# Kernel optimization log

Measured on AMD Instinct MI355X. Metric: run time of the kernel, lower is better.

## Reference

```python
import jax, jax.numpy as jnp
import numpy as np

N, E = 100000, 1600000
F_IN, H, HG, L, C = 128, 128, 128, 3, 40


def setup_inputs() -> dict:
    key = jax.random.key(0)
    ks = jax.random.split(key, 12)
    s = 0.05
    return dict(
        x=jax.random.normal(ks[0], (N, F_IN), jnp.float32),
        edge_index=jax.random.randint(ks[1], (2, E), 0, N),
        edge_weight=jax.random.uniform(ks[2], (E,), jnp.float32),
        h0=jax.random.normal(ks[3], (N, HG), jnp.float32),
        linW=jax.random.normal(ks[4], (F_IN, H), jnp.float32) * s,
        linB=jnp.zeros((H,), jnp.float32),
        convW=jax.random.normal(ks[5], (L, H, H), jnp.float32) * s,
        convB=jnp.zeros((L, H), jnp.float32),
        gru_Wih=jax.random.normal(ks[6], (3 * HG, H), jnp.float32) * s,
        gru_Whh=jax.random.normal(ks[7], (3 * HG, HG), jnp.float32) * s,
        gru_bih=jnp.zeros((3 * HG,), jnp.float32),
        gru_bhh=jnp.zeros((3 * HG,), jnp.float32),
        fcW=jax.random.normal(ks[8], (HG, C), jnp.float32) * s,
        fcB=jnp.zeros((C,), jnp.float32),
    )


def _gru(x, h, Wih, Whh, bih, bhh):
    # torch.nn.GRUCell math (gate order: r, z, n)
    gi = x @ Wih.T + bih  # [N, 3*HG]
    gh = h @ Whh.T + bhh  # [N, 3*HG]
    ir, iz, in_ = jnp.split(gi, 3, axis=-1)
    hr, hz, hn = jnp.split(gh, 3, axis=-1)
    r = jax.nn.sigmoid(ir + hr)
    z = jax.nn.sigmoid(iz + hz)
    n = jnp.tanh(in_ + r * hn)
    return (1.0 - z) * n + z * h


def _gcn_conv(x, src, dst, ew, W, b, n_nodes):
    # PyG GCNConv: linear -> symmetric-normalized sparse aggregation -> bias
    xw = x @ W  # [N, H]
    deg = jax.ops.segment_sum(ew, dst, num_segments=n_nodes)
    dinv = jnp.where(deg > 0, jax.lax.rsqrt(deg), 0.0)
    norm = dinv[src] * ew * dinv[dst]  # [E+N]
    msg = xw[src] * norm[:, None]      # gather + scale (irregular access)
    out = jax.ops.segment_sum(msg, dst, num_segments=n_nodes)  # scatter-add
    return out + b


def reference(x, edge_index, edge_weight, h0, linW, linB, convW, convB,
              gru_Wih, gru_Whh, gru_bih, gru_bhh, fcW, fcB):
    n_nodes = x.shape[0]
    # GCNConv default: add self-loops with weight 1 before normalization
    loops = jnp.arange(n_nodes)
    src = jnp.concatenate([edge_index[0], loops])
    dst = jnp.concatenate([edge_index[1], loops])
    ew = jnp.concatenate([edge_weight, jnp.ones((n_nodes,), edge_weight.dtype)])

    h = h0
    xh = jax.nn.relu(x @ linW + linB)
    h = _gru(xh, h, gru_Wih, gru_Whh, gru_bih, gru_bhh)
    for l in range(convW.shape[0]):  # fixed small layer count
        xh = jax.nn.relu(_gcn_conv(xh, src, dst, ew, convW[l], convB[l], n_nodes))
        h = _gru(xh, h, gru_Wih, gru_Whh, gru_bih, gru_bhh)
    return h @ fcW + fcB
```

## Files before the change

kernel.cpp:

```cpp
#include <hip/hip_runtime.h>
#include <hip/hip_bf16.h>
#include <math.h>

typedef __attribute__((ext_vector_type(8))) short bf8_t;
typedef __attribute__((ext_vector_type(4))) float f4_t;
typedef __attribute__((ext_vector_type(8))) unsigned short us8_t;

__device__ inline unsigned short f2bf(float f) {
  union { float f; unsigned u; } x; x.f = f;
  unsigned r = x.u + 0x7FFF + ((x.u >> 16) & 1);
  return (unsigned short)(r >> 16);
}
__device__ inline float bflo(unsigned v) {
  union { unsigned u; float f; } x; x.u = v << 16; return x.f;
}
__device__ inline float bfhi(unsigned v) {
  union { unsigned u; float f; } x; x.u = v & 0xFFFF0000u; return x.f;
}

__device__ inline void async_copy16(const void* g, void* l) {
  __builtin_amdgcn_global_load_lds(
      (const __attribute__((address_space(1))) unsigned int*)g,
      (__attribute__((address_space(3))) unsigned int*)l, 16, 0, 0);
}


__device__ inline void packB_body(const float* __restrict__ W,
                                  unsigned short* __restrict__ out,
                                  int K, int Ncols, int ldw, int trans, int bid) {
  int idx = bid * 256 + threadIdx.x;
  int total = (Ncols / 16) * (K / 32) * 64;
  if (idx >= total) return;
  int lane = idx & 63;
  int frag = idx >> 6;
  int kt = K / 32;
  int k0 = frag % kt;
  int n0 = frag / kt;
  int n = n0 * 16 + (lane & 15);
  int kbase = k0 * 32 + (lane >> 4) * 8;
  us8_t v;
#pragma unroll
  for (int j = 0; j < 8; ++j) {
    int k = kbase + j;
    float f = trans ? W[(size_t)n * ldw + k] : W[(size_t)k * ldw + n];
    v[j] = f2bf(f);
  }
  *(us8_t*)(out + (size_t)idx * 8) = v;
}

__device__ inline void fill_body(const int* __restrict__ src, const int* __restrict__ dst,
                                 const float* __restrict__ ew, const int* __restrict__ rowptr,
                                 const int* __restrict__ pos, int2* __restrict__ csr,
                                 int E, int bid) {
  int e = bid * 256 + threadIdx.x;
  if (e >= E) return;
  int d = dst[e];
  int p = rowptr[d] + pos[e];
  unsigned long long v = (unsigned long long)(unsigned)src[e] |
                         ((unsigned long long)(unsigned)__float_as_int(ew[e]) << 32);
  __builtin_nontemporal_store(v, (unsigned long long*)(csr + p));
}

__device__ inline void deg_body(const int* __restrict__ rowptr, const int2* __restrict__ csr,
                                float* __restrict__ dinv, int N, int bid) {
  int n = bid * 256 + threadIdx.x;
  if (n >= N) return;
  int b = rowptr[n], e = rowptr[n + 1];
  float s = 1.0f;
  for (int j = b; j < e; ++j) {
    unsigned long long v = __builtin_nontemporal_load((const unsigned long long*)(csr + j));
    s += __int_as_float((int)(v >> 32));
  }
  dinv[n] = rsqrtf(s);
}

__device__ inline void norm_body(const int* __restrict__ rowptr, int2* __restrict__ csr,
                                 const float* __restrict__ dinv, int N, int bid) {
  int n = bid * 256 + threadIdx.x;
  if (n >= N) return;
  int b = rowptr[n], e = rowptr[n + 1];
  float dn = dinv[n];
  for (int j = b; j < e; ++j) {
    unsigned long long v = __builtin_nontemporal_load((const unsigned long long*)(csr + j));
    int s = (int)v;
    float w = dinv[s] * __int_as_float((int)(v >> 32)) * dn;
    unsigned long long nv = (unsigned long long)(unsigned)s |
                            ((unsigned long long)(unsigned)__float_as_int(w) << 32);
    __builtin_nontemporal_store(nv, (unsigned long long*)(csr + j));
  }
}

__device__ inline void gemm_body(const unsigned short* __restrict__ A,
                                 const unsigned short* __restrict__ Bp,
                                 const float* __restrict__ bias,
                                 unsigned short* __restrict__ C, int M, int bid,
                                 bool relu, bool hasbias, unsigned char* smem) {
  int wave = threadIdx.x >> 6, lane = threadIdx.x & 63;
  int row0 = (bid * 4 + wave) * 16;
  int m = lane & 15, q = lane >> 4;

#pragma unroll
  for (int i = 0; i < 8; ++i) {
    int f = wave * 8 + i;
    async_copy16((const unsigned char*)Bp + (size_t)f * 1024 + lane * 16,
                 smem + f * 1024);
  }
  __syncthreads();
  if (row0 >= M) return;

  int arow = row0 + m; if (arow >= M) arow = M - 1;
  bf8_t a[4];
#pragma unroll
  for (int k0 = 0; k0 < 4; ++k0)
    a[k0] = *(const bf8_t*)(A + (size_t)arow * 128 + k0 * 32 + q * 8);

#pragma unroll
  for (int n0 = 0; n0 < 8; ++n0) {
    f4_t acc = {};
#pragma unroll
    for (int k0 = 0; k0 < 4; ++k0) {
      bf8_t b = *(const bf8_t*)(smem + (n0 * 4 + k0) * 1024 + lane * 16);
      acc = __builtin_amdgcn_mfma_f32_16x16x32_bf16(a[k0], b, acc, 0, 0, 0);
    }
    int col = n0 * 16 + m;
    float bs = hasbias ? bias[col] : 0.f;
#pragma unroll
    for (int r = 0; r < 4; ++r) {
      int grow = row0 + q * 4 + r;
      if (grow < M) {
        float v = acc[r] + bs;
        if (relu) v = fmaxf(v, 0.f);
        C[(size_t)grow * 128 + col] = f2bf(v);
      }
    }
  }
}

__device__ inline void gru_stage(const unsigned short* __restrict__ Bi,
                                 const unsigned short* __restrict__ Bh,
                                 unsigned char* smem, int wave, int lane, int g) {
#pragma unroll
  for (int s = 0; s < 6; ++s) {
    int cc = g + 8 * (s >= 3 ? s - 3 : s);
    const unsigned short* src = (s < 3) ? Bi : Bh;
    int f = s * 4 + wave;
    async_copy16((const unsigned char*)src + ((size_t)(cc * 4 + wave)) * 1024 + lane * 16,
                 smem + f * 1024);
  }
}

__device__ inline void gru_core(const bf8_t* ax, const float* h_in, float* h_out,
                                const unsigned short* __restrict__ Bi,
                                const unsigned short* __restrict__ Bh,
                                const float* __restrict__ bih, const float* __restrict__ bhh,
                                int M, int row0, int wave, int lane, unsigned char* smem) {
  int m = lane & 15, q = lane >> 4;
  int arow = row0 + m; if (arow >= M) arow = M - 1;

  bf8_t ah[4];
#pragma unroll
  for (int k0 = 0; k0 < 4; ++k0) {
    const float* hp = h_in + (size_t)arow * 128 + k0 * 32 + q * 8;
    float4 h0 = *(const float4*)hp;
    float4 h1 = *(const float4*)(hp + 4);
    bf8_t t;
    t[0] = (short)f2bf(h0.x); t[1] = (short)f2bf(h0.y);
    t[2] = (short)f2bf(h0.z); t[3] = (short)f2bf(h0.w);
    t[4] = (short)f2bf(h1.x); t[5] = (short)f2bf(h1.y);
    t[6] = (short)f2bf(h1.z); t[7] = (short)f2bf(h1.w);
    ah[k0] = t;
  }

  for (int g = 0; g < 8; ++g) {
    __syncthreads();
    f4_t air = {}, aiz = {}, ain = {}, ahr = {}, ahz = {}, ahn = {};
#pragma unroll
    for (int k0 = 0; k0 < 4; ++k0) {
      bf8_t br = *(const bf8_t*)(smem + (0 * 4 + k0) * 1024 + lane * 16);
      bf8_t bz = *(const bf8_t*)(smem + (1 * 4 + k0) * 1024 + lane * 16);
      bf8_t bn = *(const bf8_t*)(smem + (2 * 4 + k0) * 1024 + lane * 16);
      bf8_t cr = *(const bf8_t*)(smem + (3 * 4 + k0) * 1024 + lane * 16);
      bf8_t cz = *(const bf8_t*)(smem + (4 * 4 + k0) * 1024 + lane * 16);
      bf8_t cn = *(const bf8_t*)(smem + (5 * 4 + k0) * 1024 + lane * 16);
      air = __builtin_amdgcn_mfma_f32_16x16x32_bf16(ax[k0], br, air, 0, 0, 0);
      aiz = __builtin_amdgcn_mfma_f32_16x16x32_bf16(ax[k0], bz, aiz, 0, 0, 0);
      ain = __builtin_amdgcn_mfma_f32_16x16x32_bf16(ax[k0], bn, ain, 0, 0, 0);
      ahr = __builtin_amdgcn_mfma_f32_16x16x32_bf16(ah[k0], cr, ahr, 0, 0, 0);
      ahz = __builtin_amdgcn_mfma_f32_16x16x32_bf16(ah[k0], cz, ahz, 0, 0, 0);
      ahn = __builtin_amdgcn_mfma_f32_16x16x32_bf16(ah[k0], cn, ahn, 0, 0, 0);
    }
    __syncthreads();
    if (g < 7) gru_stage(Bi, Bh, smem, wave, lane, g + 1);

    int col = g * 16 + m;
    float bir_ = bih[col], biz_ = bih[col + 128], bin_ = bih[col + 256];
    float bhr_ = bhh[col], bhz_ = bhh[col + 128], bhn_ = bhh[col + 256];
#pragma unroll
    for (int r = 0; r < 4; ++r) {
      int grow = row0 + q * 4 + r;
      if (grow < M) {
        float hprev = h_in[(size_t)grow * 128 + col];
        float rr = 1.f / (1.f + expf(-(air[r] + bir_ + ahr[r] + bhr_)));
        float zz = 1.f / (1.f + expf(-(aiz[r] + biz_ + ahz[r] + bhz_)));
        float nn = tanhf(ain[r] + bin_ + rr * (ahn[r] + bhn_));
        h_out[(size_t)grow * 128 + col] = (1.f - zz) * nn + zz * hprev;
      }
    }
  }
}


__global__ __launch_bounds__(256) void k_prep(
    const float* __restrict__ linW, const float* __restrict__ convW,
    const float* __restrict__ Wih, const float* __restrict__ Whh,
    unsigned short* __restrict__ linWp, unsigned short* __restrict__ convWp,
    unsigned short* __restrict__ Bi, unsigned short* __restrict__ Bh,
    int* __restrict__ cnt, int N) {
  int b = blockIdx.x;
  if (b < 8)  { packB_body(linW, linWp, 128, 128, 128, 0, b); return; }
  if (b < 32) { int l = (b - 8) >> 3;
                packB_body(convW + (size_t)l * 16384, convWp + (size_t)l * 16384,
                           128, 128, 128, 0, (b - 8) & 7); return; }
  if (b < 56) { packB_body(Wih, Bi, 128, 384, 128, 1, b - 32); return; }
  if (b < 80) { packB_body(Whh, Bh, 128, 384, 128, 1, b - 56); return; }
  int i = (b - 80) * 256 + threadIdx.x;
  if (i < N) cnt[i] = 0;
}

__global__ __launch_bounds__(256) void k_count_f2bf(
    const int* __restrict__ dst, int* __restrict__ cnt, int* __restrict__ pos, int E,
    const float* __restrict__ xin, unsigned short* __restrict__ xout, size_t n8,
    int nCnt) {
  if ((int)blockIdx.x < nCnt) {
    int e = blockIdx.x * 256 + threadIdx.x;
    if (e < E) pos[e] = atomicAdd(&cnt[dst[e]], 1);
    return;
  }
  size_t i = (size_t)(blockIdx.x - nCnt) * 256 + threadIdx.x;
  if (i >= n8) return;
  const float4* p = (const float4*)(xin + i * 8);
  float4 a = p[0], b = p[1];
  us8_t v;
  v[0] = f2bf(a.x); v[1] = f2bf(a.y); v[2] = f2bf(a.z); v[3] = f2bf(a.w);
  v[4] = f2bf(b.x); v[5] = f2bf(b.y); v[6] = f2bf(b.z); v[7] = f2bf(b.w);
  *(us8_t*)(xout + i * 8) = v;
}

__global__ __launch_bounds__(256) void k_scan_block(
    const int* __restrict__ cnt, int* __restrict__ partial,
    int* __restrict__ bsum, int n) {
  __shared__ int s[256];
  int tid = threadIdx.x;
  int i = blockIdx.x * 256 + tid;
  s[tid] = (i < n) ? cnt[i] : 0;
  __syncthreads();
#pragma unroll
  for (int d = 1; d < 256; d <<= 1) {
    int t = (tid >= d) ? s[tid - d] : 0;
    __syncthreads();
    s[tid] += t;
    __syncthreads();
  }
  if (i < n) partial[i] = s[tid];
  if (tid == 255) bsum[blockIdx.x] = s[255];
}

__global__ __launch_bounds__(512) void k_scan_sums(int* __restrict__ bsum, int nb) {
  __shared__ int s[512];
  int tid = threadIdx.x;
  s[tid] = (tid < nb) ? bsum[tid] : 0;
  __syncthreads();
#pragma unroll
  for (int d = 1; d < 512; d <<= 1) {
    int t = (tid >= d) ? s[tid - d] : 0;
    __syncthreads();
    s[tid] += t;
    __syncthreads();
  }
  if (tid < nb) bsum[tid] = s[tid];
}

__global__ __launch_bounds__(256) void k_scan_add(
    const int* __restrict__ partial, const int* __restrict__ bsum,
    int* __restrict__ rowptr, int n) {
  int i = blockIdx.x * 256 + threadIdx.x;
  if (i == 0) rowptr[0] = 0;
  if (i < n) {
    int v = partial[i] + (blockIdx.x > 0 ? bsum[blockIdx.x - 1] : 0);
    rowptr[i + 1] = v;
  }
}

__global__ __launch_bounds__(256) void k_fill_lin(
    const int* __restrict__ src, const int* __restrict__ dstI,
    const float* __restrict__ ew, const int* __restrict__ rowptr,
    const int* __restrict__ pos, int2* __restrict__ csr, int E,
    const unsigned short* __restrict__ A, const unsigned short* __restrict__ Bp,
    const float* __restrict__ bias, unsigned short* __restrict__ C, int M,
    int nFill) {
  __shared__ unsigned char smem[32 * 1024];
  if ((int)blockIdx.x < nFill) {
    fill_body(src, dstI, ew, rowptr, pos, csr, E, blockIdx.x);
    return;
  }
  gemm_body(A, Bp, bias, C, M, blockIdx.x - nFill, true, true, smem);
}

__global__ __launch_bounds__(256) void k_deg_gru(
    const int* __restrict__ rowptr, const int2* __restrict__ csr,
    float* __restrict__ dinv, int N,
    const unsigned short* __restrict__ xh, const float* h_in, float* h_out,
    const unsigned short* __restrict__ Bi, const unsigned short* __restrict__ Bh,
    const float* __restrict__ bih, const float* __restrict__ bhh, int M,
    int nDeg) {
  __shared__ unsigned char smem[24 * 1024];
  if ((int)blockIdx.x < nDeg) {
    deg_body(rowptr, csr, dinv, N, blockIdx.x);
    return;
  }
  int bid = blockIdx.x - nDeg;
  int wave = threadIdx.x >> 6, lane = threadIdx.x & 63;
  int row0 = (bid * 4 + wave) * 16;
  gru_stage(Bi, Bh, smem, wave, lane, 0);
  int m = lane & 15, q = lane >> 4;
  int arow = row0 + m; if (arow >= M) arow = M - 1;
  bf8_t ax[4];
#pragma unroll
  for (int k0 = 0; k0 < 4; ++k0)
    ax[k0] = *(const bf8_t*)(xh + (size_t)arow * 128 + k0 * 32 + q * 8);
  gru_core(ax, h_in, h_out, Bi, Bh, bih, bhh, M, row0, wave, lane, smem);
}

__global__ __launch_bounds__(256) void k_norm_conv(
    const int* __restrict__ rowptr, int2* __restrict__ csr,
    const float* __restrict__ dinv, int N,
    const unsigned short* __restrict__ A, const unsigned short* __restrict__ Bp,
    unsigned short* __restrict__ C, int M, int nNorm) {
  __shared__ unsigned char smem[32 * 1024];
  if ((int)blockIdx.x < nNorm) {
    norm_body(rowptr, csr, dinv, N, blockIdx.x);
    return;
  }
  gemm_body(A, Bp, nullptr, C, M, blockIdx.x - nNorm, false, false, smem);
}

template<bool RELU, bool BIAS>
__global__ __launch_bounds__(256) void k_mfma_gemm(
    const unsigned short* __restrict__ A, const unsigned short* __restrict__ Bp,
    const float* __restrict__ bias, unsigned short* __restrict__ C, int M) {
  __shared__ unsigned char smem[32 * 1024];
  gemm_body(A, Bp, bias, C, M, blockIdx.x, RELU, BIAS, smem);
}


template<bool WRITE_XH>
__global__ __launch_bounds__(256) void k_gather_gru(
    const int* __restrict__ rowptr, const int2* __restrict__ csr,
    const unsigned* __restrict__ xw,
    const float* __restrict__ dinv, const float* __restrict__ bias,
    const float* h_in, float* h_out,
    const unsigned short* __restrict__ Bi, const unsigned short* __restrict__ Bh,
    const float* __restrict__ bih, const float* __restrict__ bhh,
    unsigned* __restrict__ xh_out, int M) {
  __shared__ unsigned char smem[24 * 1024];
  __shared__ unsigned char rows_[4][16 * 256];
  int wave = threadIdx.x >> 6, lane = threadIdx.x & 63;
  int row0 = (blockIdx.x * 4 + wave) * 16;

  gru_stage(Bi, Bh, smem, wave, lane, 0);

  float2 bb = *(const float2*)(bias + lane * 2);

  for (int j = 0; j < 16; ++j) {
    int node = row0 + j;
    unsigned o = 0u;
    if (node < M) {
      int beg = __builtin_amdgcn_readfirstlane(rowptr[node]);
      int end = __builtin_amdgcn_readfirstlane(rowptr[node + 1]);
      float accl = 0.f, acch = 0.f;
      int k = beg;
      for (; k + 4 <= end; k += 4) {
        unsigned long long r0 = __builtin_nontemporal_load((const unsigned long long*)(csr + k));
        unsigned long long r1 = __builtin_nontemporal_load((const unsigned long long*)(csr + k + 1));
        unsigned long long r2 = __builtin_nontemporal_load((const unsigned long long*)(csr + k + 2));
        unsigned long long r3 = __builtin_nontemporal_load((const unsigned long long*)(csr + k + 3));
        unsigned v0 = xw[((size_t)(unsigned)r0 << 6) + lane];
        unsigned v1 = xw[((size_t)(unsigned)r1 << 6) + lane];
        unsigned v2 = xw[((size_t)(unsigned)r2 << 6) + lane];
        unsigned v3 = xw[((size_t)(unsigned)r3 << 6) + lane];
        float w0 = __int_as_float((int)(r0 >> 32)), w1 = __int_as_float((int)(r1 >> 32));
        float w2 = __int_as_float((int)(r2 >> 32)), w3 = __int_as_float((int)(r3 >> 32));
        accl += bflo(v0) * w0; acch += bfhi(v0) * w0;
        accl += bflo(v1) * w1; acch += bfhi(v1) * w1;
        accl += bflo(v2) * w2; acch += bfhi(v2) * w2;
        accl += bflo(v3) * w3; acch += bfhi(v3) * w3;
      }
      for (; k < end; ++k) {
        unsigned long long r = __builtin_nontemporal_load((const unsigned long long*)(csr + k));
        unsigned v = xw[((size_t)(unsigned)r << 6) + lane];
        float w = __int_as_float((int)(r >> 32));
        accl += bflo(v) * w; acch += bfhi(v) * w;
      }
      float di = dinv[node];
      float sn = di * di;
      unsigned vs = xw[((size_t)node << 6) + lane];
      float rl = fmaxf(accl + bflo(vs) * sn + bb.x, 0.f);
      float rh = fmaxf(acch + bfhi(vs) * sn + bb.y, 0.f);
      o = (unsigned)f2bf(rl) | ((unsigned)f2bf(rh) << 16);
      if (WRITE_XH) xh_out[((size_t)node << 6) + lane] = o;
    }
    unsigned byteoff = ((unsigned)(lane * 4)) ^ (((unsigned)(j & 7)) << 4);
    *(unsigned*)(&rows_[wave][j * 256] + byteoff) = o;
  }

  int m = lane & 15, q = lane >> 4;
  bf8_t ax[4];
#pragma unroll
  for (int k0 = 0; k0 < 4; ++k0) {
    unsigned rb = ((unsigned)(k0 * 64 + q * 16)) ^ (((unsigned)(m & 7)) << 4);
    ax[k0] = *(const bf8_t*)(&rows_[wave][m * 256] + rb);
  }
  gru_core(ax, h_in, h_out, Bi, Bh, bih, bhh, M, row0, wave, lane, smem);
}


template<bool RELU, bool BIAS>
__global__ __launch_bounds__(256) void k_gemm128(
    const float* __restrict__ A, const float* __restrict__ B,
    const float* __restrict__ bias, float* __restrict__ C, int M, int Nc) {
  __shared__ float As[64][36];
  __shared__ float Bs[32][64];
  int tid = threadIdx.x;
  int tx = tid & 15, ty = tid >> 4;
  int row0 = blockIdx.y * 64, col0 = blockIdx.x * 64;
  float acc[4][4] = {};

  for (int k0 = 0; k0 < 128; k0 += 32) {
#pragma unroll
    for (int i = 0; i < 2; ++i) {
      int f = tid + i * 256;
      int r = f >> 3, c4 = f & 7;
      int gr = row0 + r;
      float4 v = make_float4(0.f, 0.f, 0.f, 0.f);
      if (gr < M) v = *(const float4*)(A + (size_t)gr * 128 + k0 + c4 * 4);
      *(float4*)(&As[r][c4 * 4]) = v;
    }
#pragma unroll
    for (int i = 0; i < 2; ++i) {
      int f = tid + i * 256;
      int r = f >> 4, c4 = f & 15;
      int gc = col0 + c4 * 4;
      float4 v = make_float4(0.f, 0.f, 0.f, 0.f);
      if (gc + 3 < Nc) v = *(const float4*)(B + (size_t)(k0 + r) * Nc + gc);
      *(float4*)(&Bs[r][c4 * 4]) = v;
    }
    __syncthreads();
#pragma unroll
    for (int kk = 0; kk < 32; ++kk) {
      float4 b = *(float4*)(&Bs[kk][tx * 4]);
      float a0 = As[ty * 4 + 0][kk];
      float a1 = As[ty * 4 + 1][kk];
      float a2 = As[ty * 4 + 2][kk];
      float a3 = As[ty * 4 + 3][kk];
      acc[0][0] += a0 * b.x; acc[0][1] += a0 * b.y; acc[0][2] += a0 * b.z; acc[0][3] += a0 * b.w;
      acc[1][0] += a1 * b.x; acc[1][1] += a1 * b.y; acc[1][2] += a1 * b.z; acc[1][3] += a1 * b.w;
      acc[2][0] += a2 * b.x; acc[2][1] += a2 * b.y; acc[2][2] += a2 * b.z; acc[2][3] += a2 * b.w;
      acc[3][0] += a3 * b.x; acc[3][1] += a3 * b.y; acc[3][2] += a3 * b.z; acc[3][3] += a3 * b.w;
    }
    __syncthreads();
  }

#pragma unroll
  for (int i = 0; i < 4; ++i) {
    int gr = row0 + ty * 4 + i;
    if (gr >= M) continue;
#pragma unroll
    for (int j = 0; j < 4; ++j) {
      int gc = col0 + tx * 4 + j;
      if (gc >= Nc) continue;
      float v = acc[i][j];
      if (BIAS) v += bias[gc];
      if (RELU) v = fmaxf(v, 0.f);
      C[(size_t)gr * Nc + gc] = v;
    }
  }
}


extern "C" void kernel_launch(void* const* d_in, const int* in_sizes, int n_in,
                              void* d_out, int out_size, void* d_ws, size_t ws_size,
                              hipStream_t stream) {
  const float* x    = (const float*)d_in[0];
  const int*   ei   = (const int*)d_in[1];
  const float* ew   = (const float*)d_in[2];
  const float* h0   = (const float*)d_in[3];
  const float* linW = (const float*)d_in[4];
  const float* linB = (const float*)d_in[5];
  const float* convW= (const float*)d_in[6];
  const float* convB= (const float*)d_in[7];
  const float* Wih  = (const float*)d_in[8];
  const float* Whh  = (const float*)d_in[9];
  const float* bih  = (const float*)d_in[10];
  const float* bhh  = (const float*)d_in[11];
  const float* fcW  = (const float*)d_in[12];
  const float* fcB  = (const float*)d_in[13];

  int N = in_sizes[0] / 128;
  int E = in_sizes[1] / 2;
  const int* srcI = ei;
  const int* dstI = ei + E;
  int nb = (N + 255) / 256;

  float* ws = (float*)d_ws;
  size_t off = 0;
  float* dinv = ws + off; off += (size_t)N;
  if (off & 1) off++;
  float* h    = ws + off; off += (size_t)N * 128;
  int* iws = (int*)(ws + off);
  size_t ioff = 0;
  int2* csr    = (int2*)iws; ioff += (size_t)2 * E;
  int* cnt     = iws + ioff; ioff += (size_t)N;
  int* partial = iws + ioff; ioff += (size_t)N;
  int* bsum    = iws + ioff; ioff += 512;
  int* rowptr  = iws + ioff; ioff += (size_t)N + 1;
  ioff = (ioff + 3) & ~(size_t)3;
  unsigned short* usws = (unsigned short*)(iws + ioff);
  size_t uoff = 0;
  unsigned short* x_bf   = usws + uoff; uoff += (size_t)N * 128;
  unsigned short* xh_bf  = usws + uoff; uoff += (size_t)N * 128;
  unsigned short* xw_bf  = usws + uoff; uoff += (size_t)N * 128;
  unsigned short* linWp  = usws + uoff; uoff += 128 * 128;
  unsigned short* convWp = usws + uoff; uoff += 3 * 128 * 128;
  unsigned short* Bi     = usws + uoff; uoff += 384 * 128;
  unsigned short* Bh     = usws + uoff; uoff += 384 * 128;

  int* pos = (int*)xw_bf;

  int gwave = (N + 63) / 64;
  int nCnt  = (E + 255) / 256;
  int nF2   = (int)(((size_t)N * 16 + 255) / 256);

  k_prep<<<80 + nb, 256, 0, stream>>>(linW, convW, Wih, Whh,
                                      linWp, convWp, Bi, Bh, cnt, N);
  k_count_f2bf<<<nCnt + nF2, 256, 0, stream>>>(dstI, cnt, pos, E,
                                               x, x_bf, (size_t)N * 16, nCnt);
  k_scan_block<<<nb, 256, 0, stream>>>(cnt, partial, bsum, N);
  k_scan_sums<<<1, 512, 0, stream>>>(bsum, nb);
  k_scan_add<<<nb, 256, 0, stream>>>(partial, bsum, rowptr, N);
  k_fill_lin<<<nCnt + gwave, 256, 0, stream>>>(srcI, dstI, ew, rowptr, pos, csr, E,
                                               x_bf, linWp, linB, xh_bf, N, nCnt);
  k_deg_gru<<<nb + gwave, 256, 0, stream>>>(rowptr, csr, dinv, N,
                                            xh_bf, h0, h, Bi, Bh, bih, bhh, N, nb);
  k_norm_conv<<<nb + gwave, 256, 0, stream>>>(rowptr, csr, dinv, N,
                                              xh_bf, convWp, xw_bf, N, nb);
  k_gather_gru<true><<<gwave, 256, 0, stream>>>(
      rowptr, csr, (const unsigned*)xw_bf, dinv, convB,
      h, h, Bi, Bh, bih, bhh, (unsigned*)xh_bf, N);
  k_mfma_gemm<false, false><<<gwave, 256, 0, stream>>>(
      xh_bf, convWp + (size_t)1 * 128 * 128, nullptr, xw_bf, N);
  k_gather_gru<true><<<gwave, 256, 0, stream>>>(
      rowptr, csr, (const unsigned*)xw_bf, dinv, convB + 128,
      h, h, Bi, Bh, bih, bhh, (unsigned*)xh_bf, N);
  k_mfma_gemm<false, false><<<gwave, 256, 0, stream>>>(
      xh_bf, convWp + (size_t)2 * 128 * 128, nullptr, xw_bf, N);
  k_gather_gru<false><<<gwave, 256, 0, stream>>>(
      rowptr, csr, (const unsigned*)xw_bf, dinv, convB + 256,
      h, h, Bi, Bh, bih, bhh, nullptr, N);
  dim3 g40(1, (N + 63) / 64);
  k_gemm128<false, true><<<g40, 256, 0, stream>>>(h, fcW, fcB, (float*)d_out, N, 40);
}
```

Measured before the change: 986.4 us.

## Split gather from GRU and co-schedule GRU with next-layer conv GEMM

Result: no change. 976.9 us (-1.0%).

```diff
diff --git a/kernel.cpp b/kernel.cpp
--- a/kernel.cpp
+++ b/kernel.cpp
@@ -207,6 +207,24 @@
       }
     }
   }
+}
+
+__device__ inline void gru_body(const unsigned short* __restrict__ xh,
+                                const float* h_in, float* h_out,
+                                const unsigned short* __restrict__ Bi,
+                                const unsigned short* __restrict__ Bh,
+                                const float* __restrict__ bih, const float* __restrict__ bhh,
+                                int M, int bid, unsigned char* smem) {
+  int wave = threadIdx.x >> 6, lane = threadIdx.x & 63;
+  int row0 = (bid * 4 + wave) * 16;
+  gru_stage(Bi, Bh, smem, wave, lane, 0);
+  int m = lane & 15, q = lane >> 4;
+  int arow = row0 + m; if (arow >= M) arow = M - 1;
+  bf8_t ax[4];
+#pragma unroll
+  for (int k0 = 0; k0 < 4; ++k0)
+    ax[k0] = *(const bf8_t*)(xh + (size_t)arow * 128 + k0 * 32 + q * 8);
+  gru_core(ax, h_in, h_out, Bi, Bh, bih, bhh, M, row0, wave, lane, smem);
 }
 
 
@@ -318,17 +336,7 @@
     deg_body(rowptr, csr, dinv, N, blockIdx.x);
     return;
   }
-  int bid = blockIdx.x - nDeg;
-  int wave = threadIdx.x >> 6, lane = threadIdx.x & 63;
-  int row0 = (bid * 4 + wave) * 16;
-  gru_stage(Bi, Bh, smem, wave, lane, 0);
-  int m = lane & 15, q = lane >> 4;
-  int arow = row0 + m; if (arow >= M) arow = M - 1;
-  bf8_t ax[4];
-#pragma unroll
-  for (int k0 = 0; k0 < 4; ++k0)
-    ax[k0] = *(const bf8_t*)(xh + (size_t)arow * 128 + k0 * 32 + q * 8);
-  gru_core(ax, h_in, h_out, Bi, Bh, bih, bhh, M, row0, wave, lane, smem);
+  gru_body(xh, h_in, h_out, Bi, Bh, bih, bhh, M, blockIdx.x - nDeg, smem);
 }
 
 __global__ __launch_bounds__(256) void k_norm_conv(
@@ -344,83 +352,74 @@
   gemm_body(A, Bp, nullptr, C, M, blockIdx.x - nNorm, false, false, smem);
 }
 
-template<bool RELU, bool BIAS>
-__global__ __launch_bounds__(256) void k_mfma_gemm(
-    const unsigned short* __restrict__ A, const unsigned short* __restrict__ Bp,
-    const float* __restrict__ bias, unsigned short* __restrict__ C, int M) {
+__global__ __launch_bounds__(256) void k_gru_conv(
+    const unsigned short* __restrict__ xh, const float* h_in, float* h_out,
+    const unsigned short* __restrict__ Bi, const unsigned short* __restrict__ Bh,
+    const float* __restrict__ bih, const float* __restrict__ bhh,
+    const unsigned short* __restrict__ Bp, unsigned short* __restrict__ xw,
+    int M, int nGru) {
   __shared__ unsigned char smem[32 * 1024];
-  gemm_body(A, Bp, bias, C, M, blockIdx.x, RELU, BIAS, smem);
-}
-
-
-template<bool WRITE_XH>
-__global__ __launch_bounds__(256) void k_gather_gru(
+  if ((int)blockIdx.x < nGru) {
+    gru_body(xh, h_in, h_out, Bi, Bh, bih, bhh, M, blockIdx.x, smem);
+    return;
+  }
+  gemm_body(xh, Bp, nullptr, xw, M, blockIdx.x - nGru, false, false, smem);
+}
+
+__global__ __launch_bounds__(256) void k_gru(
+    const unsigned short* __restrict__ xh, const float* h_in, float* h_out,
+    const unsigned short* __restrict__ Bi, const unsigned short* __restrict__ Bh,
+    const float* __restrict__ bih, const float* __restrict__ bhh, int M) {
+  __shared__ unsigned char smem[24 * 1024];
+  gru_body(xh, h_in, h_out, Bi, Bh, bih, bhh, M, blockIdx.x, smem);
+}
+
+
+__global__ __launch_bounds__(256) void k_gather(
     const int* __restrict__ rowptr, const int2* __restrict__ csr,
     const unsigned* __restrict__ xw,
     const float* __restrict__ dinv, const float* __restrict__ bias,
-    const float* h_in, float* h_out,
-    const unsigned short* __restrict__ Bi, const unsigned short* __restrict__ Bh,
-    const float* __restrict__ bih, const float* __restrict__ bhh,
-    unsigned* __restrict__ xh_out, int M) {
-  __shared__ unsigned char smem[24 * 1024];
-  __shared__ unsigned char rows_[4][16 * 256];
-  int wave = threadIdx.x >> 6, lane = threadIdx.x & 63;
-  int row0 = (blockIdx.x * 4 + wave) * 16;
-
-  gru_stage(Bi, Bh, smem, wave, lane, 0);
-
-  float2 bb = *(const float2*)(bias + lane * 2);
-
-  for (int j = 0; j < 16; ++j) {
-    int node = row0 + j;
-    unsigned o = 0u;
-    if (node < M) {
-      int beg = __builtin_amdgcn_readfirstlane(rowptr[node]);
-      int end = __builtin_amdgcn_readfirstlane(rowptr[node + 1]);
-      float accl = 0.f, acch = 0.f;
-      int k = beg;
-      for (; k + 4 <= end; k += 4) {
-        unsigned long long r0 = __builtin_nontemporal_load((const unsigned long long*)(csr + k));
-        unsigned long long r1 = __builtin_nontemporal_load((const unsigned long long*)(csr + k + 1));
-        unsigned long long r2 = __builtin_nontemporal_load((const unsigned long long*)(csr + k + 2));
-        unsigned long long r3 = __builtin_nontemporal_load((const unsigned long long*)(csr + k + 3));
-        unsigned v0 = xw[((size_t)(unsigned)r0 << 6) + lane];
-        unsigned v1 = xw[((size_t)(unsigned)r1 << 6) + lane];
-        unsigned v2 = xw[((size_t)(unsigned)r2 << 6) + lane];
-        unsigned v3 = xw[((size_t)(unsigned)r3 << 6) + lane];
-        float w0 = __int_as_float((int)(r0 >> 32)), w1 = __int_as_float((int)(r1 >> 32));
-        float w2 = __int_as_float((int)(r2 >> 32)), w3 = __int_as_float((int)(r3 >> 32));
-        accl += bflo(v0) * w0; acch += bfhi(v0) * w0;
-        accl += bflo(v1) * w1; acch += bfhi(v1) * w1;
-        accl += bflo(v2) * w2; acch += bfhi(v2) * w2;
-        accl += bflo(v3) * w3; acch += bfhi(v3) * w3;
-      }
-      for (; k < end; ++k) {
-        unsigned long long r = __builtin_nontemporal_load((const unsigned long long*)(csr + k));
-        unsigned v = xw[((size_t)(unsigned)r << 6) + lane];
-        float w = __int_as_float((int)(r >> 32));
-        accl += bflo(v) * w; acch += bfhi(v) * w;
-      }
-      float di = dinv[node];
-      float sn = di * di;
-      unsigned vs = xw[((size_t)node << 6) + lane];
-      float rl = fmaxf(accl + bflo(vs) * sn + bb.x, 0.f);
-      float rh = fmaxf(acch + bfhi(vs) * sn + bb.y, 0.f);
-      o = (unsigned)f2bf(rl) | ((unsigned)f2bf(rh) << 16);
-      if (WRITE_XH) xh_out[((size_t)node << 6) + lane] = o;
-    }
-    unsigned byteoff = ((unsigned)(lane * 4)) ^ (((unsigned)(j & 7)) << 4);
-    *(unsigned*)(&rows_[wave][j * 256] + byteoff) = o;
-  }
-
-  int m = lane & 15, q = lane >> 4;
-  bf8_t ax[4];
-#pragma unroll
-  for (int k0 = 0; k0 < 4; ++k0) {
-    unsigned rb = ((unsigned)(k0 * 64 + q * 16)) ^ (((unsigned)(m & 7)) << 4);
-    ax[k0] = *(const bf8_t*)(&rows_[wave][m * 256] + rb);
-  }
-  gru_core(ax, h_in, h_out, Bi, Bh, bih, bhh, M, row0, wave, lane, smem);
+    unsigned* __restrict__ out, int N) {
+  int wave = threadIdx.x >> 6;
+  int lane = threadIdx.x & 63;
+  int node = __builtin_amdgcn_readfirstlane(blockIdx.x * 4 + wave);
+  if (node >= N) return;
+  int beg = __builtin_amdgcn_readfirstlane(rowptr[node]);
+  int end = __builtin_amdgcn_readfirstlane(rowptr[node + 1]);
+
+  float accl = 0.f, acch = 0.f;
+  int k = beg;
+  for (; k + 4 <= end; k += 4) {
+    unsigned long long r0 = __builtin_nontemporal_load((const unsigned long long*)(csr + k));
+    unsigned long long r1 = __builtin_nontemporal_load((const unsigned long long*)(csr + k + 1));
+    unsigned long long r2 = __builtin_nontemporal_load((const unsigned long long*)(csr + k + 2));
+    unsigned long long r3 = __builtin_nontemporal_load((const unsigned long long*)(csr + k + 3));
+    unsigned v0 = xw[((size_t)(unsigned)r0 << 6) + lane];
+    unsigned v1 = xw[((size_t)(unsigned)r1 << 6) + lane];
+    unsigned v2 = xw[((size_t)(unsigned)r2 << 6) + lane];
+    unsigned v3 = xw[((size_t)(unsigned)r3 << 6) + lane];
+    float w0 = __int_as_float((int)(r0 >> 32)), w1 = __int_as_float((int)(r1 >> 32));
+    float w2 = __int_as_float((int)(r2 >> 32)), w3 = __int_as_float((int)(r3 >> 32));
+    accl += bflo(v0) * w0; acch += bfhi(v0) * w0;
+    accl += bflo(v1) * w1; acch += bfhi(v1) * w1;
+    accl += bflo(v2) * w2; acch += bfhi(v2) * w2;
+    accl += bflo(v3) * w3; acch += bfhi(v3) * w3;
+  }
+  for (; k < end; ++k) {
+    unsigned long long r = __builtin_nontemporal_load((const unsigned long long*)(csr + k));
+    unsigned v = xw[((size_t)(unsigned)r << 6) + lane];
+    float w = __int_as_float((int)(r >> 32));
+    accl += bflo(v) * w; acch += bfhi(v) * w;
+  }
+
+  float di = dinv[node];
+  float sn = di * di;
+  unsigned vs = xw[((size_t)node << 6) + lane];
+  float2 b = *(const float2*)(bias + lane * 2);
+  float rl = fmaxf(accl + bflo(vs) * sn + b.x, 0.f);
+  float rh = fmaxf(acch + bfhi(vs) * sn + b.y, 0.f);
+  unsigned o = (unsigned)f2bf(rl) | ((unsigned)f2bf(rh) << 16);
+  out[((size_t)node << 6) + lane] = o;
 }
 
 
@@ -553,19 +552,21 @@
                                             xh_bf, h0, h, Bi, Bh, bih, bhh, N, nb);
   k_norm_conv<<<nb + gwave, 256, 0, stream>>>(rowptr, csr, dinv, N,
                                               xh_bf, convWp, xw_bf, N, nb);
-  k_gather_gru<true><<<gwave, 256, 0, stream>>>(
-      rowptr, csr, (const unsigned*)xw_bf, dinv, convB,
-      h, h, Bi, Bh, bih, bhh, (unsigned*)xh_bf, N);
-  k_mfma_gemm<false, false><<<gwave, 256, 0, stream>>>(
-      xh_bf, convWp + (size_t)1 * 128 * 128, nullptr, xw_bf, N);
-  k_gather_gru<true><<<gwave, 256, 0, stream>>>(
-      rowptr, csr, (const unsigned*)xw_bf, dinv, convB + 128,
-      h, h, Bi, Bh, bih, bhh, (unsigned*)xh_bf, N);
-  k_mfma_gemm<false, false><<<gwave, 256, 0, stream>>>(
-      xh_bf, convWp + (size_t)2 * 128 * 128, nullptr, xw_bf, N);
-  k_gather_gru<false><<<gwave, 256, 0, stream>>>(
-      rowptr, csr, (const unsigned*)xw_bf, dinv, convB + 256,
-      h, h, Bi, Bh, bih, bhh, nullptr, N);
+
+  int ggat = (N + 3) / 4;
+  k_gather<<<ggat, 256, 0, stream>>>(rowptr, csr, (const unsigned*)xw_bf, dinv,
+                                     convB, (unsigned*)xh_bf, N);
+  k_gru_conv<<<2 * gwave, 256, 0, stream>>>(
+      xh_bf, h, h, Bi, Bh, bih, bhh,
+      convWp + (size_t)1 * 128 * 128, xw_bf, N, gwave);
+  k_gather<<<ggat, 256, 0, stream>>>(rowptr, csr, (const unsigned*)xw_bf, dinv,
+                                     convB + 128, (unsigned*)xh_bf, N);
+  k_gru_conv<<<2 * gwave, 256, 0, stream>>>(
+      xh_bf, h, h, Bi, Bh, bih, bhh,
+      convWp + (size_t)2 * 128 * 128, xw_bf, N, gwave);
+  k_gather<<<ggat, 256, 0, stream>>>(rowptr, csr, (const unsigned*)xw_bf, dinv,
+                                     convB + 256, (unsigned*)xh_bf, N);
+  k_gru<<<gwave, 256, 0, stream>>>(xh_bf, h, h, Bi, Bh, bih, bhh, N);
   dim3 g40(1, (N + 63) / 64);
   k_gemm128<false, true><<<g40, 256, 0, stream>>>(h, fcW, fcB, (float*)d_out, N, 40);
 }
```
